# Kernel tuning notes

Measured on AMD Instinct MI355X. Metric: run time of the kernel, lower is better.

## Reference

```python
import jax, jax.numpy as jnp
import numpy as np

D_MODEL = 1024
D_INNER = 2048
D_STATE = 16
D_CONV = 4
DT_RANK = 64
BATCH = 2
SEQLEN = 1024


def setup_inputs() -> dict:
    key = jax.random.key(0)
    ks = jax.random.split(key, 12)
    s = 0.02
    # dt bias initialized as inverse-softplus of dt ~ LogUniform(1e-3, 1e-1), as in the torch code
    dt = jnp.exp(jax.random.uniform(ks[7], (D_INNER,)) * (np.log(0.1) - np.log(0.001)) + np.log(0.001))
    dt = jnp.clip(dt, 1e-4, None)
    inv_dt = jnp.log(jnp.expm1(dt))
    A_log = jnp.log(jnp.broadcast_to(jnp.arange(1, D_STATE + 1, dtype=jnp.float32), (D_INNER, D_STATE)))
    return {
        "hidden_states": jax.random.normal(ks[0], (BATCH, SEQLEN, D_MODEL), jnp.float32),
        "x_text": jax.random.normal(ks[1], (BATCH, D_MODEL), jnp.float32),
        "in_proj_w": jax.random.normal(ks[2], (2 * D_INNER, D_MODEL), jnp.float32) * s,
        "conv_w": jax.random.normal(ks[3], (D_INNER, 1, D_CONV), jnp.float32) * s,
        "conv_b": jax.random.normal(ks[4], (D_INNER,), jnp.float32) * s,
        "x_proj_w": jax.random.normal(ks[5], (DT_RANK + 2 * D_STATE, D_INNER), jnp.float32) * s,
        "dt_proj_w": jax.random.normal(ks[6], (D_INNER, DT_RANK), jnp.float32) * (DT_RANK ** -0.5),
        "dt_proj_b": inv_dt.astype(jnp.float32),
        "A_log": A_log.astype(jnp.float32),
        "D": jnp.ones((D_INNER,), jnp.float32),
        "out_proj_w": jax.random.normal(ks[8], (D_MODEL, D_INNER), jnp.float32) * s,
        "gate_w": jax.random.normal(ks[9], (DT_RANK + 2 * D_STATE, D_MODEL), jnp.float32) * s,
        "gate_b": jnp.zeros((DT_RANK + 2 * D_STATE,), jnp.float32),
    }


def _causal_depthwise_conv(x, w, b):
    # x: (b, d, l), w: (d, 1, k) depthwise, left-pad k-1 for causality
    y = jax.lax.conv_general_dilated(
        x, w, window_strides=(1,), padding=[(D_CONV - 1, 0)],
        dimension_numbers=("NCH", "OIH", "NCH"), feature_group_count=D_INNER)
    return y + b[None, :, None]


def _mamba_forward(hidden_states, x_text, in_proj_w, conv_w, conv_b, x_proj_w,
                   dt_proj_w, dt_proj_b, A_log, D, out_proj_w, gate_w, gate_b):
    b = hidden_states.shape[0]
    # input projection -> x, z each (b, l, d_inner)
    xz = jnp.einsum("bld,ed->ble", hidden_states, in_proj_w)
    x, z = jnp.split(xz, 2, axis=-1)
    # causal depthwise conv + SiLU
    xc = _causal_depthwise_conv(jnp.transpose(x, (0, 2, 1)), conv_w, conv_b)
    xc = jnp.transpose(jax.nn.silu(xc), (0, 2, 1))  # (b, l, d_inner)
    # x_proj -> dt/B/C, modulated by text gate
    x_dbl = jnp.einsum("bld,ed->ble", xc, x_proj_w)  # (b, l, dt_rank+2n)
    gate = jax.nn.sigmoid(x_text @ gate_w.T + gate_b)  # (b, dt_rank+2n)
    x_dbl = x_dbl * gate[:, None, :]
    dt, Bm, Cm = jnp.split(x_dbl, [DT_RANK, DT_RANK + D_STATE], axis=-1)
    delta = jax.nn.softplus(jnp.einsum("blr,dr->bld", dt, dt_proj_w) + dt_proj_b)  # (b, l, d)
    A = -jnp.exp(A_log)  # (d, n)
    dA = jnp.exp(jnp.einsum("bld,dn->bldn", delta, A))          # (b, l, d, n)
    dBx = jnp.einsum("bld,bln->bldn", delta * xc, Bm)            # (b, l, d, n)

    def step(h, inp):
        dA_t, dBx_t, C_t = inp
        h = h * dA_t + dBx_t                       # (b, d, n)
        y_t = jnp.einsum("bdn,bn->bd", h, C_t)
        return h, y_t

    h0 = jnp.zeros((b, D_INNER, D_STATE), delta.dtype)
    _, ys = jax.lax.scan(step, h0, (jnp.transpose(dA, (1, 0, 2, 3)),
                                    jnp.transpose(dBx, (1, 0, 2, 3)),
                                    jnp.transpose(Cm, (1, 0, 2))))
    y = jnp.transpose(ys, (1, 0, 2)) + D * xc      # (b, l, d_inner)
    y = y * jax.nn.silu(z)
    return jnp.einsum("bld,md->blm", y, out_proj_w)


def reference(hidden_states, x_text, in_proj_w, conv_w, conv_b, x_proj_w,
              dt_proj_w, dt_proj_b, A_log, D, out_proj_w, gate_w, gate_b):
    return _mamba_forward(hidden_states, x_text, in_proj_w, conv_w, conv_b, x_proj_w,
                          dt_proj_w, dt_proj_b, A_log, D, out_proj_w, gate_w, gate_b)
```

## Files before the change

### kernel.cpp

```cpp
#include <hip/hip_runtime.h>

#define BATCH   2
#define SEQLEN  1024
#define DMODEL  1024
#define DINNER  2048
#define DSTATE  16
#define DCONV   4
#define DTRANK  64
#define GDIM    96
#define MROWS   (BATCH*SEQLEN)

#define NCHUNK  64
#define LCHUNK  16
#define SPLITX  32

typedef __attribute__((ext_vector_type(8))) short bf16x8_t;
typedef __attribute__((ext_vector_type(4))) float f32x4_t;
typedef __attribute__((ext_vector_type(4))) unsigned short u16x4_t;
typedef unsigned short ushort_t;

__device__ __forceinline__ unsigned short f2bf(float x) {
    union { float f; unsigned int u; } v; v.f = x;
    unsigned int r = v.u + 0x7FFFu + ((v.u >> 16) & 1u);
    return (unsigned short)(r >> 16);
}
__device__ __forceinline__ float bf2f(unsigned short h) {
    union { unsigned int u; float f; } v; v.u = ((unsigned int)h) << 16;
    return v.f;
}

__device__ __forceinline__ void gload_lds16(const ushort_t* g, short* l) {
    __builtin_amdgcn_global_load_lds(
        (const __attribute__((address_space(1))) unsigned int*)g,
        (__attribute__((address_space(3))) unsigned int*)l, 16, 0, 0);
}

#define N1 (MROWS*DMODEL)
#define N2 (2*DINNER*DMODEL)
#define N3 (GDIM*DINNER)
#define N4 (DINNER*DTRANK)
#define N5 (DMODEL*DINNER)
#define NTOT (N1+N2+N3+N4+N5)
__global__ __launch_bounds__(256)
void cvt5_kernel(const float* __restrict__ s1, const float* __restrict__ s2,
                 const float* __restrict__ s3, const float* __restrict__ s4,
                 const float* __restrict__ s5,
                 ushort_t* o1, ushort_t* o2, ushort_t* o3, ushort_t* o4, ushort_t* o5) {
    int idx = (blockIdx.x * 256 + threadIdx.x) * 4;
    if (idx >= NTOT) return;
    const float* src; ushort_t* dst;
    if (idx < N1)              { src = s1; dst = o1; }
    else if ((idx -= N1) < N2) { src = s2; dst = o2; }
    else if ((idx -= N2) < N3) { src = s3; dst = o3; }
    else if ((idx -= N3) < N4) { src = s4; dst = o4; }
    else                       { idx -= N4; src = s5; dst = o5; }
    f32x4_t v = *(const f32x4_t*)(src + idx);
    u16x4_t o;
    #pragma unroll
    for (int j = 0; j < 4; j++) o[j] = f2bf(v[j]);
    *(u16x4_t*)(dst + idx) = o;
}

template<int EPI>
__global__ __launch_bounds__(256)
void gemm_bf(const ushort_t* __restrict__ A, const ushort_t* __restrict__ W,
             void* __restrict__ out0, void* __restrict__ out1,
             const float* __restrict__ bias, int M, int N, int K) {
    __shared__ __align__(16) short As[128 * 32];
    __shared__ __align__(16) short Bs[128 * 32];

    const int tid  = threadIdx.x;
    const int m0   = blockIdx.x * 128;
    const int n0   = blockIdx.y * 128;
    const int klen = K / gridDim.z;
    const int kbeg = blockIdx.z * klen;

    const int w    = tid >> 6;
    const int lane = tid & 63;
    const int quad = lane >> 4;
    const int l15  = lane & 15;
    const int wm   = (w >> 1) * 64;
    const int wn   = (w & 1) * 64;

    const int rA0 = (w * 2 + 0) * 16 + (lane >> 2);
    const int rA1 = (w * 2 + 1) * 16 + (lane >> 2);
    const int kc  = (lane & 3) * 8;
    const int arow0 = m0 + rA0;
    const int arow1 = m0 + rA1;
    int brow0 = n0 + rA0; if (brow0 > N - 1) brow0 = N - 1;
    int brow1 = n0 + rA1; if (brow1 > N - 1) brow1 = N - 1;

    f32x4_t acc[4][4];
    #pragma unroll
    for (int i = 0; i < 4; i++)
        #pragma unroll
        for (int j = 0; j < 4; j++)
            acc[i][j] = (f32x4_t){0.f, 0.f, 0.f, 0.f};

    for (int k0 = 0; k0 < klen; k0 += 32) {
        const int kk = kbeg + k0 + kc;
        __syncthreads();
        gload_lds16(A + (size_t)arow0 * K + kk, &As[(w * 2 + 0) * 512]);
        gload_lds16(A + (size_t)arow1 * K + kk, &As[(w * 2 + 1) * 512]);
        gload_lds16(W + (size_t)brow0 * K + kk, &Bs[(w * 2 + 0) * 512]);
        gload_lds16(W + (size_t)brow1 * K + kk, &Bs[(w * 2 + 1) * 512]);
        __syncthreads();

        bf16x8_t af[4], bfv[4];
        #pragma unroll
        for (int mi = 0; mi < 4; mi++)
            af[mi] = *(const bf16x8_t*)(&As[(wm + mi * 16 + l15) * 32 + quad * 8]);
        #pragma unroll
        for (int ni = 0; ni < 4; ni++)
            bfv[ni] = *(const bf16x8_t*)(&Bs[(wn + ni * 16 + l15) * 32 + quad * 8]);
        #pragma unroll
        for (int mi = 0; mi < 4; mi++)
            #pragma unroll
            for (int ni = 0; ni < 4; ni++)
                acc[mi][ni] = __builtin_amdgcn_mfma_f32_16x16x32_bf16(af[mi], bfv[ni], acc[mi][ni], 0, 0, 0);
    }

    const size_t zoff = (size_t)blockIdx.z * M * N;
    #pragma unroll
    for (int mi = 0; mi < 4; mi++) {
        #pragma unroll
        for (int ni = 0; ni < 4; ni++) {
            #pragma unroll
            for (int r = 0; r < 4; r++) {
                int gm = m0 + wm + mi * 16 + quad * 4 + r;
                int gn = n0 + wn + ni * 16 + l15;
                if (gn < N) {
                    float v = acc[mi][ni][r];
                    if (EPI == 0) {
                        ((float*)out0)[zoff + (size_t)gm * N + gn] = v;
                    } else if (EPI == 1) {
                        float t = v + bias[gn];
                        float sp = (t > 20.f) ? t : log1pf(__expf(t));
                        ((ushort_t*)out0)[(size_t)gm * N + gn] = f2bf(sp);
                    } else {
                        if (gn < DINNER)
                            ((float*)out0)[(size_t)gm * DINNER + gn] = v;
                        else
                            ((float*)out1)[(size_t)gm * DINNER + (gn - DINNER)] = v;
                    }
                }
            }
        }
    }
}

#define CONVBLK ((MROWS*DINNER)/256)
__global__ __launch_bounds__(256)
void convgate_kernel(const float* __restrict__ x,
                     const float* __restrict__ cw,
                     const float* __restrict__ cb,
                     ushort_t* __restrict__ xc,
                     const float* __restrict__ xt,
                     const float* __restrict__ gw,
                     const float* __restrict__ gb,
                     float* __restrict__ gate) {
    if (blockIdx.x < CONVBLK) {
        int idx = blockIdx.x * 256 + threadIdx.x;
        int d  = idx & (DINNER - 1);
        int bl = idx >> 11;
        int l  = bl & (SEQLEN - 1);
        float acc = cb[d];
        #pragma unroll
        for (int j = 0; j < DCONV; j++) {
            int lj = l - (DCONV - 1) + j;
            if (lj >= 0)
                acc += cw[d * DCONV + j] * x[(size_t)(bl - (DCONV - 1) + j) * DINNER + d];
        }
        float v = acc / (1.f + __expf(-acc));
        xc[idx] = f2bf(v);
    } else {
        int g = blockIdx.x - CONVBLK;
        int b = g / GDIM, j = g % GDIM;
        int tid = threadIdx.x;
        float s = 0.f;
        for (int k = tid; k < DMODEL; k += 256)
            s += xt[b * DMODEL + k] * gw[j * DMODEL + k];
        #pragma unroll
        for (int o = 32; o > 0; o >>= 1) s += __shfl_down(s, o);
        __shared__ float red[4];
        if ((tid & 63) == 0) red[tid >> 6] = s;
        __syncthreads();
        if (tid == 0) {
            float t = red[0] + red[1] + red[2] + red[3] + gb[j];
            gate[b * GDIM + j] = 1.f / (1.f + __expf(-t));
        }
    }
}

__global__ void gatemul_kernel(const float* __restrict__ xp,
                               const float* __restrict__ gate,
                               ushort_t* __restrict__ dt,
                               float* __restrict__ Bm,
                               float* __restrict__ Cm) {
    int idx = blockIdx.x * 256 + threadIdx.x;
    if (idx >= MROWS * GDIM) return;
    int j  = idx % GDIM;
    int bl = idx / GDIM;
    int b  = bl >> 10;
    float v = 0.f;
    #pragma unroll
    for (int z = 0; z < SPLITX; z++)
        v += xp[(size_t)z * MROWS * GDIM + idx];
    v *= gate[b * GDIM + j];
    if (j < DTRANK)               dt[bl * DTRANK + j] = f2bf(v);
    else if (j < DTRANK + DSTATE) Bm[bl * DSTATE + (j - DTRANK)] = v;
    else                          Cm[bl * DSTATE + (j - DTRANK - DSTATE)] = v;
}

__global__ __launch_bounds__(256)
void scan1_kernel(const ushort_t* __restrict__ delta,
                  const ushort_t* __restrict__ xc,
                  const float* __restrict__ Bm,
                  const float* __restrict__ A_log,
                  float* __restrict__ hfin,
                  float* __restrict__ aprod) {
    __shared__ float sBm[LCHUNK][DSTATE];
    int tid = threadIdx.x;
    int d = blockIdx.x * 256 + tid;
    int b = blockIdx.y;
    int c = blockIdx.z;
    int l0 = c * LCHUNK;
    for (int t = tid; t < LCHUNK * DSTATE; t += 256)
        sBm[t >> 4][t & 15] = Bm[((size_t)(b * SEQLEN + l0 + (t >> 4))) * DSTATE + (t & 15)];
    __syncthreads();

    float Ac[DSTATE];
    #pragma unroll
    for (int n = 0; n < DSTATE; n++)
        Ac[n] = -__expf(A_log[d * DSTATE + n]);
    float h[DSTATE], p[DSTATE];
    #pragma unroll
    for (int n = 0; n < DSTATE; n++) { h[n] = 0.f; p[n] = 1.f; }

    for (int s = 0; s < LCHUNK; s++) {
        size_t ix = (size_t)(b * SEQLEN + l0 + s) * DINNER + d;
        float dv = bf2f(delta[ix]);
        float xv = bf2f(xc[ix]);
        float dx = dv * xv;
        #pragma unroll
        for (int n = 0; n < DSTATE; n++) {
            float e = __expf(dv * Ac[n]);
            h[n] = h[n] * e + dx * sBm[s][n];
            p[n] *= e;
        }
    }
    size_t base = ((size_t)(b * DINNER + d) * NCHUNK + c) * DSTATE;
    #pragma unroll
    for (int n = 0; n < DSTATE; n++) { hfin[base + n] = h[n]; aprod[base + n] = p[n]; }
}

__global__ __launch_bounds__(256)
void scan2_kernel(float* __restrict__ hfin,
                  const float* __restrict__ aprod) {
    __shared__ float sh[NCHUNK * DSTATE];
    __shared__ float sp[NCHUNK * DSTATE];
    const int tid = threadIdx.x;
    const size_t base = (size_t)blockIdx.x * (NCHUNK * DSTATE);
    #pragma unroll
    for (int r = 0; r < 4; r++) {
        int i = tid + r * 256;
        sh[i] = hfin[base + i];
        sp[i] = aprod[base + i];
    }
    __syncthreads();
    #pragma unroll
    for (int s = 1; s < NCHUNK; s <<= 1) {
        float nh[4], np[4];
        #pragma unroll
        for (int r = 0; r < 4; r++) {
            int i = tid + r * 256;
            int c = i >> 4;
            if (c >= s) {
                int j = i - (s << 4);
                nh[r] = sh[i] + sp[i] * sh[j];
                np[r] = sp[i] * sp[j];
            } else { nh[r] = sh[i]; np[r] = sp[i]; }
        }
        __syncthreads();
        #pragma unroll
        for (int r = 0; r < 4; r++) { int i = tid + r * 256; sh[i] = nh[r]; sp[i] = np[r]; }
        __syncthreads();
    }
    #pragma unroll
    for (int r = 0; r < 4; r++) {
        int i = tid + r * 256;
        hfin[base + i] = (i >> 4) ? sh[i - 16] : 0.f;
    }
}

__global__ __launch_bounds__(256)
void scan3_kernel(const ushort_t* __restrict__ delta,
                  ushort_t* __restrict__ xc,
                  const float* __restrict__ z,
                  const float* __restrict__ Bm,
                  const float* __restrict__ Cm,
                  const float* __restrict__ A_log,
                  const float* __restrict__ Dp,
                  const float* __restrict__ h0) {
    __shared__ float sBm[LCHUNK][DSTATE];
    __shared__ float sCm[LCHUNK][DSTATE];
    int tid = threadIdx.x;
    int d = blockIdx.x * 256 + tid;
    int b = blockIdx.y;
    int c = blockIdx.z;
    int l0 = c * LCHUNK;
    for (int t = tid; t < LCHUNK * DSTATE; t += 256) {
        size_t src = ((size_t)(b * SEQLEN + l0 + (t >> 4))) * DSTATE + (t & 15);
        sBm[t >> 4][t & 15] = Bm[src];
        sCm[t >> 4][t & 15] = Cm[src];
    }
    __syncthreads();

    float Ac[DSTATE];
    #pragma unroll
    for (int n = 0; n < DSTATE; n++)
        Ac[n] = -__expf(A_log[d * DSTATE + n]);

    float h[DSTATE];
    size_t hb0 = ((size_t)(b * DINNER + d) * NCHUNK + c) * DSTATE;
    #pragma unroll
    for (int n = 0; n < DSTATE; n++) h[n] = h0[hb0 + n];

    float Dv = Dp[d];

    for (int s = 0; s < LCHUNK; s++) {
        size_t ix = (size_t)(b * SEQLEN + l0 + s) * DINNER + d;
        float dv = bf2f(delta[ix]);
        float xv = bf2f(xc[ix]);
        float dx = dv * xv;
        float y = 0.f;
        #pragma unroll
        for (int n = 0; n < DSTATE; n++) {
            float e = __expf(dv * Ac[n]);
            h[n] = h[n] * e + dx * sBm[s][n];
            y += h[n] * sCm[s][n];
        }
        float zv = z[ix];
        float o = (y + Dv * xv) * (zv / (1.f + __expf(-zv)));
        xc[ix] = f2bf(o);
    }
}

__global__ void reduce4_kernel(const float* __restrict__ p, float* __restrict__ out, int n) {
    int i = blockIdx.x * 256 + threadIdx.x;
    if (i < n)
        out[i] = (p[i] + p[(size_t)n + i]) + (p[2 * (size_t)n + i] + p[3 * (size_t)n + i]);
}

extern "C" void kernel_launch(void* const* d_in, const int* in_sizes, int n_in,
                              void* d_out, int out_size, void* d_ws, size_t ws_size,
                              hipStream_t stream) {
    const float* hidden   = (const float*)d_in[0];
    const float* x_text   = (const float*)d_in[1];
    const float* in_proj  = (const float*)d_in[2];
    const float* conv_w   = (const float*)d_in[3];
    const float* conv_b   = (const float*)d_in[4];
    const float* x_proj   = (const float*)d_in[5];
    const float* dt_proj  = (const float*)d_in[6];
    const float* dt_bias  = (const float*)d_in[7];
    const float* A_log    = (const float*)d_in[8];
    const float* Dparam   = (const float*)d_in[9];
    const float* out_proj = (const float*)d_in[10];
    const float* gate_w   = (const float*)d_in[11];
    const float* gate_b   = (const float*)d_in[12];

    char* ws = (char*)d_ws;
    size_t off = 0;
    auto alloc = [&](size_t bytes) -> char* {
        char* p = ws + off;
        off += (bytes + 255) & ~(size_t)255;
        return p;
    };
    ushort_t* hb    = (ushort_t*)alloc((size_t)N1 * 2);
    ushort_t* w_in  = (ushort_t*)alloc((size_t)N2 * 2);
    ushort_t* w_x   = (ushort_t*)alloc((size_t)N3 * 2);
    ushort_t* w_dt  = (ushort_t*)alloc((size_t)N4 * 2);
    ushort_t* w_o   = (ushort_t*)alloc((size_t)N5 * 2);
    float*    X     = (float*)alloc((size_t)MROWS * DINNER * 4);
    float*    zbuf  = (float*)alloc((size_t)MROWS * DINNER * 4);
    float*    hfin  = (float*)alloc((size_t)BATCH * DINNER * NCHUNK * DSTATE * 4);
    float*    aprod = (float*)alloc((size_t)BATCH * DINNER * NCHUNK * DSTATE * 4);
    float*    gate  = (float*)alloc((size_t)BATCH * GDIM * 4);
    float*    Bm    = (float*)alloc((size_t)MROWS * DSTATE * 4);
    float*    Cm    = (float*)alloc((size_t)MROWS * DSTATE * 4);
    ushort_t* dt    = (ushort_t*)alloc((size_t)MROWS * DTRANK * 2);

    ushort_t* xc     = w_in;
    float*    xdbl_p = hfin;
    ushort_t* delta  = (ushort_t*)X;
    float*    outp   = X;

    cvt5_kernel<<<(NTOT / 4 + 255) / 256, 256, 0, stream>>>(
        hidden, in_proj, x_proj, dt_proj, out_proj, hb, w_in, w_x, w_dt, w_o);

    gemm_bf<3><<<dim3(MROWS / 128, (2 * DINNER) / 128, 1), 256, 0, stream>>>(
        hb, w_in, X, zbuf, nullptr, MROWS, 2 * DINNER, DMODEL);

    convgate_kernel<<<CONVBLK + BATCH * GDIM, 256, 0, stream>>>(
        X, conv_w, conv_b, xc, x_text, gate_w, gate_b, gate);

    gemm_bf<0><<<dim3(MROWS / 128, 1, SPLITX), 256, 0, stream>>>(
        xc, w_x, xdbl_p, nullptr, nullptr, MROWS, GDIM, DINNER);

    gatemul_kernel<<<(MROWS * GDIM + 255) / 256, 256, 0, stream>>>(
        xdbl_p, gate, dt, Bm, Cm);

    gemm_bf<1><<<dim3(MROWS / 128, DINNER / 128, 1), 256, 0, stream>>>(
        dt, w_dt, delta, nullptr, dt_bias, MROWS, DINNER, DTRANK);

    scan1_kernel<<<dim3(DINNER / 256, BATCH, NCHUNK), 256, 0, stream>>>(
        delta, xc, Bm, A_log, hfin, aprod);

    scan2_kernel<<<BATCH * DINNER, 256, 0, stream>>>(hfin, aprod);

    scan3_kernel<<<dim3(DINNER / 256, BATCH, NCHUNK), 256, 0, stream>>>(
        delta, xc, zbuf, Bm, Cm, A_log, Dparam, hfin);

    gemm_bf<0><<<dim3(MROWS / 128, DMODEL / 128, 4), 256, 0, stream>>>(
        xc, w_o, outp, nullptr, nullptr, MROWS, DMODEL, DINNER);

    reduce4_kernel<<<(MROWS * DMODEL + 255) / 256, 256, 0, stream>>>(
        outp, (float*)d_out, MROWS * DMODEL);
}
```

Before: 293.8 us.

## Double-buffer GEMM LDS with XOR swizzle, atomic split-K, and cheaper scan carry

The GEMM gets double-buffered LDS tiles with one barrier per k-step, and an XOR swizzle on the k-chunk to reduce LDS bank conflicts. Split-K GEMMs now accumulate with float atomics into zeroed outputs, which removes the partial buffers and the separate reduce kernel. The zeroing is folded into the conversion kernel. The scan stores a per-chunk sum of delta instead of 16 per-state decay products, and the second pass recomputes the products as exp(A*sum), which cuts memory traffic. Atomic accumulation makes the sum order nondeterministic and adds atomic contention.

```diff
diff --git a/kernel.cpp b/kernel.cpp
--- a/kernel.cpp
+++ b/kernel.cpp
@@ -41,24 +41,36 @@
 #define N4 (DINNER*DTRANK)
 #define N5 (DMODEL*DINNER)
 #define NTOT (N1+N2+N3+N4+N5)
-__global__ __launch_bounds__(256)
-void cvt5_kernel(const float* __restrict__ s1, const float* __restrict__ s2,
-                 const float* __restrict__ s3, const float* __restrict__ s4,
-                 const float* __restrict__ s5,
-                 ushort_t* o1, ushort_t* o2, ushort_t* o3, ushort_t* o4, ushort_t* o5) {
-    int idx = (blockIdx.x * 256 + threadIdx.x) * 4;
-    if (idx >= NTOT) return;
-    const float* src; ushort_t* dst;
-    if (idx < N1)              { src = s1; dst = o1; }
-    else if ((idx -= N1) < N2) { src = s2; dst = o2; }
-    else if ((idx -= N2) < N3) { src = s3; dst = o3; }
-    else if ((idx -= N3) < N4) { src = s4; dst = o4; }
-    else                       { idx -= N4; src = s5; dst = o5; }
-    f32x4_t v = *(const f32x4_t*)(src + idx);
-    u16x4_t o;
-    #pragma unroll
-    for (int j = 0; j < 4; j++) o[j] = f2bf(v[j]);
-    *(u16x4_t*)(dst + idx) = o;
+#define CVTN (NTOT/4)
+#define Z1   (MROWS*DMODEL/4)
+#define Z2   (MROWS*GDIM/4)
+#define CVTBLK ((CVTN + Z1 + Z2) / 256)
+__global__ __launch_bounds__(256)
+void cvt5z_kernel(const float* __restrict__ s1, const float* __restrict__ s2,
+                  const float* __restrict__ s3, const float* __restrict__ s4,
+                  const float* __restrict__ s5,
+                  ushort_t* o1, ushort_t* o2, ushort_t* o3, ushort_t* o4, ushort_t* o5,
+                  float* __restrict__ z1, float* __restrict__ z2) {
+    int t = blockIdx.x * 256 + threadIdx.x;
+    if (t < CVTN) {
+        int idx = t * 4;
+        const float* src; ushort_t* dst;
+        if (idx < N1)              { src = s1; dst = o1; }
+        else if ((idx -= N1) < N2) { src = s2; dst = o2; }
+        else if ((idx -= N2) < N3) { src = s3; dst = o3; }
+        else if ((idx -= N3) < N4) { src = s4; dst = o4; }
+        else                       { idx -= N4; src = s5; dst = o5; }
+        f32x4_t v = *(const f32x4_t*)(src + idx);
+        u16x4_t o;
+        #pragma unroll
+        for (int j = 0; j < 4; j++) o[j] = f2bf(v[j]);
+        *(u16x4_t*)(dst + idx) = o;
+    } else if ((t -= CVTN) < Z1) {
+        ((f32x4_t*)z1)[t] = (f32x4_t){0.f, 0.f, 0.f, 0.f};
+    } else {
+        t -= Z1;
+        ((f32x4_t*)z2)[t] = (f32x4_t){0.f, 0.f, 0.f, 0.f};
+    }
 }
 
 template<int EPI>
@@ -66,8 +78,8 @@
 void gemm_bf(const ushort_t* __restrict__ A, const ushort_t* __restrict__ W,
              void* __restrict__ out0, void* __restrict__ out1,
              const float* __restrict__ bias, int M, int N, int K) {
-    __shared__ __align__(16) short As[128 * 32];
-    __shared__ __align__(16) short Bs[128 * 32];
+    __shared__ __align__(16) short As[2][128 * 32];
+    __shared__ __align__(16) short Bs[2][128 * 32];
 
     const int tid  = threadIdx.x;
     const int m0   = blockIdx.x * 128;
@@ -84,7 +96,7 @@
 
     const int rA0 = (w * 2 + 0) * 16 + (lane >> 2);
     const int rA1 = (w * 2 + 1) * 16 + (lane >> 2);
-    const int kc  = (lane & 3) * 8;
+    const int kc  = (((lane & 3) ^ ((lane >> 2) & 3)) << 3);
     const int arow0 = m0 + rA0;
     const int arow1 = m0 + rA1;
     int brow0 = n0 + rA0; if (brow0 > N - 1) brow0 = N - 1;
@@ -97,30 +109,44 @@
         for (int j = 0; j < 4; j++)
             acc[i][j] = (f32x4_t){0.f, 0.f, 0.f, 0.f};
 
+    {
+        const int kk = kbeg + kc;
+        gload_lds16(A + (size_t)arow0 * K + kk, &As[0][(w * 2 + 0) * 512]);
+        gload_lds16(A + (size_t)arow1 * K + kk, &As[0][(w * 2 + 1) * 512]);
+        gload_lds16(W + (size_t)brow0 * K + kk, &Bs[0][(w * 2 + 0) * 512]);
+        gload_lds16(W + (size_t)brow1 * K + kk, &Bs[0][(w * 2 + 1) * 512]);
+    }
+    __syncthreads();
+
+    int cur = 0;
     for (int k0 = 0; k0 < klen; k0 += 32) {
-        const int kk = kbeg + k0 + kc;
-        __syncthreads();
-        gload_lds16(A + (size_t)arow0 * K + kk, &As[(w * 2 + 0) * 512]);
-        gload_lds16(A + (size_t)arow1 * K + kk, &As[(w * 2 + 1) * 512]);
-        gload_lds16(W + (size_t)brow0 * K + kk, &Bs[(w * 2 + 0) * 512]);
-        gload_lds16(W + (size_t)brow1 * K + kk, &Bs[(w * 2 + 1) * 512]);
-        __syncthreads();
-
+        if (k0 + 32 < klen) {
+            const int kk = kbeg + k0 + 32 + kc;
+            gload_lds16(A + (size_t)arow0 * K + kk, &As[cur ^ 1][(w * 2 + 0) * 512]);
+            gload_lds16(A + (size_t)arow1 * K + kk, &As[cur ^ 1][(w * 2 + 1) * 512]);
+            gload_lds16(W + (size_t)brow0 * K + kk, &Bs[cur ^ 1][(w * 2 + 0) * 512]);
+            gload_lds16(W + (size_t)brow1 * K + kk, &Bs[cur ^ 1][(w * 2 + 1) * 512]);
+        }
         bf16x8_t af[4], bfv[4];
         #pragma unroll
-        for (int mi = 0; mi < 4; mi++)
-            af[mi] = *(const bf16x8_t*)(&As[(wm + mi * 16 + l15) * 32 + quad * 8]);
-        #pragma unroll
-        for (int ni = 0; ni < 4; ni++)
-            bfv[ni] = *(const bf16x8_t*)(&Bs[(wn + ni * 16 + l15) * 32 + quad * 8]);
+        for (int mi = 0; mi < 4; mi++) {
+            int row = wm + mi * 16 + l15;
+            af[mi] = *(const bf16x8_t*)(&As[cur][row * 32 + ((quad ^ (row & 3)) << 3)]);
+        }
+        #pragma unroll
+        for (int ni = 0; ni < 4; ni++) {
+            int row = wn + ni * 16 + l15;
+            bfv[ni] = *(const bf16x8_t*)(&Bs[cur][row * 32 + ((quad ^ (row & 3)) << 3)]);
+        }
         #pragma unroll
         for (int mi = 0; mi < 4; mi++)
             #pragma unroll
             for (int ni = 0; ni < 4; ni++)
                 acc[mi][ni] = __builtin_amdgcn_mfma_f32_16x16x32_bf16(af[mi], bfv[ni], acc[mi][ni], 0, 0, 0);
-    }
-
-    const size_t zoff = (size_t)blockIdx.z * M * N;
+        __syncthreads();
+        cur ^= 1;
+    }
+
     #pragma unroll
     for (int mi = 0; mi < 4; mi++) {
         #pragma unroll
@@ -131,17 +157,17 @@
                 int gn = n0 + wn + ni * 16 + l15;
                 if (gn < N) {
                     float v = acc[mi][ni][r];
-                    if (EPI == 0) {
-                        ((float*)out0)[zoff + (size_t)gm * N + gn] = v;
-                    } else if (EPI == 1) {
+                    if (EPI == 1) {
                         float t = v + bias[gn];
                         float sp = (t > 20.f) ? t : log1pf(__expf(t));
                         ((ushort_t*)out0)[(size_t)gm * N + gn] = f2bf(sp);
-                    } else {
+                    } else if (EPI == 3) {
                         if (gn < DINNER)
                             ((float*)out0)[(size_t)gm * DINNER + gn] = v;
                         else
                             ((float*)out1)[(size_t)gm * DINNER + (gn - DINNER)] = v;
+                    } else {
+                        atomicAdd(&((float*)out0)[(size_t)gm * N + gn], v);
                     }
                 }
             }
@@ -202,11 +228,7 @@
     int j  = idx % GDIM;
     int bl = idx / GDIM;
     int b  = bl >> 10;
-    float v = 0.f;
-    #pragma unroll
-    for (int z = 0; z < SPLITX; z++)
-        v += xp[(size_t)z * MROWS * GDIM + idx];
-    v *= gate[b * GDIM + j];
+    float v = xp[idx] * gate[b * GDIM + j];
     if (j < DTRANK)               dt[bl * DTRANK + j] = f2bf(v);
     else if (j < DTRANK + DSTATE) Bm[bl * DSTATE + (j - DTRANK)] = v;
     else                          Cm[bl * DSTATE + (j - DTRANK - DSTATE)] = v;
@@ -218,7 +240,7 @@
                   const float* __restrict__ Bm,
                   const float* __restrict__ A_log,
                   float* __restrict__ hfin,
-                  float* __restrict__ aprod) {
+                  float* __restrict__ dsum) {
     __shared__ float sBm[LCHUNK][DSTATE];
     int tid = threadIdx.x;
     int d = blockIdx.x * 256 + tid;
@@ -233,39 +255,53 @@
     #pragma unroll
     for (int n = 0; n < DSTATE; n++)
         Ac[n] = -__expf(A_log[d * DSTATE + n]);
-    float h[DSTATE], p[DSTATE];
-    #pragma unroll
-    for (int n = 0; n < DSTATE; n++) { h[n] = 0.f; p[n] = 1.f; }
+    float h[DSTATE];
+    #pragma unroll
+    for (int n = 0; n < DSTATE; n++) h[n] = 0.f;
+    float ds = 0.f;
 
     for (int s = 0; s < LCHUNK; s++) {
         size_t ix = (size_t)(b * SEQLEN + l0 + s) * DINNER + d;
         float dv = bf2f(delta[ix]);
         float xv = bf2f(xc[ix]);
         float dx = dv * xv;
+        ds += dv;
         #pragma unroll
         for (int n = 0; n < DSTATE; n++) {
             float e = __expf(dv * Ac[n]);
             h[n] = h[n] * e + dx * sBm[s][n];
-            p[n] *= e;
         }
     }
     size_t base = ((size_t)(b * DINNER + d) * NCHUNK + c) * DSTATE;
     #pragma unroll
-    for (int n = 0; n < DSTATE; n++) { hfin[base + n] = h[n]; aprod[base + n] = p[n]; }
+    for (int n = 0; n < DSTATE; n++) hfin[base + n] = h[n];
+    dsum[((size_t)b * NCHUNK + c) * DINNER + d] = ds;
 }
 
 __global__ __launch_bounds__(256)
 void scan2_kernel(float* __restrict__ hfin,
-                  const float* __restrict__ aprod) {
+                  const float* __restrict__ dsum,
+                  const float* __restrict__ A_log) {
     __shared__ float sh[NCHUNK * DSTATE];
     __shared__ float sp[NCHUNK * DSTATE];
+    __shared__ float sAc[DSTATE];
+    __shared__ float sds[NCHUNK];
     const int tid = threadIdx.x;
-    const size_t base = (size_t)blockIdx.x * (NCHUNK * DSTATE);
+    const int bd  = blockIdx.x;
+    const int b   = bd >> 11;
+    const int d   = bd & (DINNER - 1);
+    if (tid < DSTATE) sAc[tid] = -__expf(A_log[d * DSTATE + tid]);
+    if (tid < NCHUNK) sds[tid] = dsum[((size_t)b * NCHUNK + tid) * DINNER + d];
+    const size_t base = (size_t)bd * (NCHUNK * DSTATE);
+    float hl[4];
+    #pragma unroll
+    for (int r = 0; r < 4; r++) hl[r] = hfin[base + tid + r * 256];
+    __syncthreads();
     #pragma unroll
     for (int r = 0; r < 4; r++) {
         int i = tid + r * 256;
-        sh[i] = hfin[base + i];
-        sp[i] = aprod[base + i];
+        sh[i] = hl[r];
+        sp[i] = __expf(sAc[i & 15] * sds[i >> 4]);
     }
     __syncthreads();
     #pragma unroll
@@ -346,12 +382,6 @@
     }
 }
 
-__global__ void reduce4_kernel(const float* __restrict__ p, float* __restrict__ out, int n) {
-    int i = blockIdx.x * 256 + threadIdx.x;
-    if (i < n)
-        out[i] = (p[i] + p[(size_t)n + i]) + (p[2 * (size_t)n + i] + p[3 * (size_t)n + i]);
-}
-
 extern "C" void kernel_launch(void* const* d_in, const int* in_sizes, int n_in,
                               void* d_out, int out_size, void* d_ws, size_t ws_size,
                               hipStream_t stream) {
@@ -384,19 +414,19 @@
     float*    X     = (float*)alloc((size_t)MROWS * DINNER * 4);
     float*    zbuf  = (float*)alloc((size_t)MROWS * DINNER * 4);
     float*    hfin  = (float*)alloc((size_t)BATCH * DINNER * NCHUNK * DSTATE * 4);
-    float*    aprod = (float*)alloc((size_t)BATCH * DINNER * NCHUNK * DSTATE * 4);
+    float*    dsum  = (float*)alloc((size_t)BATCH * NCHUNK * DINNER * 4);
+    float*    xdbl  = (float*)alloc((size_t)MROWS * GDIM * 4);
     float*    gate  = (float*)alloc((size_t)BATCH * GDIM * 4);
     float*    Bm    = (float*)alloc((size_t)MROWS * DSTATE * 4);
     float*    Cm    = (float*)alloc((size_t)MROWS * DSTATE * 4);
     ushort_t* dt    = (ushort_t*)alloc((size_t)MROWS * DTRANK * 2);
 
-    ushort_t* xc     = w_in;
-    float*    xdbl_p = hfin;
-    ushort_t* delta  = (ushort_t*)X;
-    float*    outp   = X;
-
-    cvt5_kernel<<<(NTOT / 4 + 255) / 256, 256, 0, stream>>>(
-        hidden, in_proj, x_proj, dt_proj, out_proj, hb, w_in, w_x, w_dt, w_o);
+    ushort_t* xc    = w_in;
+    ushort_t* delta = (ushort_t*)X;
+
+    cvt5z_kernel<<<CVTBLK, 256, 0, stream>>>(
+        hidden, in_proj, x_proj, dt_proj, out_proj, hb, w_in, w_x, w_dt, w_o,
+        (float*)d_out, xdbl);
 
     gemm_bf<3><<<dim3(MROWS / 128, (2 * DINNER) / 128, 1), 256, 0, stream>>>(
         hb, w_in, X, zbuf, nullptr, MROWS, 2 * DINNER, DMODEL);
@@ -404,26 +434,23 @@
     convgate_kernel<<<CONVBLK + BATCH * GDIM, 256, 0, stream>>>(
         X, conv_w, conv_b, xc, x_text, gate_w, gate_b, gate);
 
-    gemm_bf<0><<<dim3(MROWS / 128, 1, SPLITX), 256, 0, stream>>>(
-        xc, w_x, xdbl_p, nullptr, nullptr, MROWS, GDIM, DINNER);
+    gemm_bf<4><<<dim3(MROWS / 128, 1, SPLITX), 256, 0, stream>>>(
+        xc, w_x, xdbl, nullptr, nullptr, MROWS, GDIM, DINNER);
 
     gatemul_kernel<<<(MROWS * GDIM + 255) / 256, 256, 0, stream>>>(
-        xdbl_p, gate, dt, Bm, Cm);
+        xdbl, gate, dt, Bm, Cm);
 
     gemm_bf<1><<<dim3(MROWS / 128, DINNER / 128, 1), 256, 0, stream>>>(
         dt, w_dt, delta, nullptr, dt_bias, MROWS, DINNER, DTRANK);
 
     scan1_kernel<<<dim3(DINNER / 256, BATCH, NCHUNK), 256, 0, stream>>>(
-        delta, xc, Bm, A_log, hfin, aprod);
-
-    scan2_kernel<<<BATCH * DINNER, 256, 0, stream>>>(hfin, aprod);
+        delta, xc, Bm, A_log, hfin, dsum);
+
+    scan2_kernel<<<BATCH * DINNER, 256, 0, stream>>>(hfin, dsum, A_log);
 
     scan3_kernel<<<dim3(DINNER / 256, BATCH, NCHUNK), 256, 0, stream>>>(
         delta, xc, zbuf, Bm, Cm, A_log, Dparam, hfin);
 
-    gemm_bf<0><<<dim3(MROWS / 128, DMODEL / 128, 4), 256, 0, stream>>>(
-        xc, w_o, outp, nullptr, nullptr, MROWS, DMODEL, DINNER);
-
-    reduce4_kernel<<<(MROWS * DMODEL + 255) / 256, 256, 0, stream>>>(
-        outp, (float*)d_out, MROWS * DMODEL);
-}
+    gemm_bf<4><<<dim3(MROWS / 128, DMODEL / 128, 4), 256, 0, stream>>>(
+        xc, w_o, (float*)d_out, nullptr, nullptr, MROWS, DMODEL, DINNER);
+}
```

New measurement: 308.9 us. 5.1% more time.
